# Kernel tuning notes

Measured on AMD Instinct MI355X. Metric: run time of the kernel, lower is better.

Reference implementation:

```python
import jax, jax.numpy as jnp
import numpy as np

HIDDEN_SIZE = 256
INPUT_SIZE = 4
N_CLASSES = 2
START_VALUE_PADDING = -100.0


def setup_inputs() -> dict:
    key = jax.random.key(0)
    ks = jax.random.split(key, 11)
    B, T = 128, 2048
    H, IN = HIDDEN_SIZE, INPUT_SIZE
    s = 1.0 / np.sqrt(H)  # torch LSTM/Linear default init scale
    u = lambda k, shape: jax.random.uniform(k, shape, jnp.float32, -s, s)
    return {
        "y": jax.random.normal(ks[0], (B, T), dtype=jnp.float32),
        "W_ih0": u(ks[1], (4 * H, IN)),
        "W_hh0": u(ks[2], (4 * H, H)),
        "b_ih0": u(ks[3], (4 * H,)),
        "b_hh0": u(ks[4], (4 * H,)),
        "W_ih1": u(ks[5], (4 * H, H)),
        "W_hh1": u(ks[6], (4 * H, H)),
        "b_ih1": u(ks[7], (4 * H,)),
        "b_hh1": u(ks[8], (4 * H,)),
        "W_fc": u(ks[9], (N_CLASSES, H)),
        "b_fc": u(ks[10], (N_CLASSES,)),
    }


def _cell(x, h, c, W_ih, W_hh, b):
    # torch LSTM gate order: i, f, g, o
    g = x @ W_ih.T + h @ W_hh.T + b
    i, f, gg, o = jnp.split(g, 4, axis=-1)
    c = jax.nn.sigmoid(f) * c + jax.nn.sigmoid(i) * jnp.tanh(gg)
    h = jax.nn.sigmoid(o) * jnp.tanh(c)
    return h, c


def reference(y, W_ih0, W_hh0, b_ih0, b_hh0, W_ih1, W_hh1, b_ih1, b_hh1, W_fc, b_fc):
    B, T = y.shape
    H, IN = HIDDEN_SIZE, INPUT_SIZE
    # torch roll-on-padded-array windowing == prepend IN-1 pad values,
    # window t = [y_pre[t], ..., y_pre[t+IN-1]] (oldest-first, current sample last)
    y_pre = jnp.concatenate(
        [jnp.full((B, IN - 1), START_VALUE_PADDING, y.dtype), y], axis=1)
    idx = jnp.arange(T)[:, None] + jnp.arange(IN)[None, :]  # [T, IN]
    seq = y_pre[:, idx]  # [B, T, IN]

    b0 = b_ih0 + b_hh0
    b1 = b_ih1 + b_hh1

    def step(carry, x_t):
        h1, c1, h2, c2 = carry
        h1, c1 = _cell(x_t, h1, c1, W_ih0, W_hh0, b0)
        h2, c2 = _cell(h1, h2, c2, W_ih1, W_hh1, b1)
        return (h1, c1, h2, c2), h2

    z = jnp.zeros((B, H), y.dtype)
    _, hs = jax.lax.scan(step, (z, z, z, z), seq.transpose(1, 0, 2))  # hs: [T,B,H]
    lstm_out = hs.transpose(1, 0, 2)  # [B, T, H]
    out = lstm_out @ W_fc.T + b_fc  # [B, T, N_CLASSES]  (phase='train')
    return out
```

## Files before the change

### kernel.cpp

```cpp
#include <hip/hip_runtime.h>
#include <math.h>

#define T_LEN 2048
#define NTH   512

typedef __attribute__((ext_vector_type(8))) short short8v;
typedef __attribute__((ext_vector_type(4))) float f32x4;
typedef unsigned int u32t;
typedef unsigned long long u64t;

#define H1_OFF  0
#define H2_OFF  131072
#define ABT_OFF 262144
#define WS_U32  262145


__device__ __forceinline__ float fsigm(float x) {
  return __builtin_amdgcn_rcpf(1.0f + __builtin_amdgcn_exp2f(-1.44269504f * x));
}
__device__ __forceinline__ float ftanh(float x) {
  return fmaf(-2.0f, __builtin_amdgcn_rcpf(1.0f + __builtin_amdgcn_exp2f(2.88539009f * x)), 1.0f);
}
__device__ __forceinline__ u32t bf_rn(float x) {
  u32t b; __builtin_memcpy(&b, &x, 4);
  return (b + 0x7FFFu + ((b >> 16) & 1u)) >> 16;
}
__device__ __forceinline__ void split_bf(float x, u32t& hi, u32t& lo) {
  hi = bf_rn(x);
  u32t hb = hi << 16; float hf; __builtin_memcpy(&hf, &hb, 4);
  lo = bf_rn(x - hf);
}

__global__ void init_ws_kernel(u32t* ws) {
  for (int i = blockIdx.x * blockDim.x + threadIdx.x; i < WS_U32;
       i += gridDim.x * blockDim.x)
    ws[i] = (i < ABT_OFF) ? 0x40000000u : 0u;
}

#define MFMA16(a, b, c) __builtin_amdgcn_mfma_f32_16x16x32_bf16(a, b, c, 0, 0, 0)
#define ALD64(ptr) __hip_atomic_load((ptr), __ATOMIC_RELAXED, __HIP_MEMORY_SCOPE_AGENT)
#define ALD32(ptr) __hip_atomic_load((ptr), __ATOMIC_RELAXED, __HIP_MEMORY_SCOPE_AGENT)
#define AST32(ptr, v) __hip_atomic_store((ptr), (v), __ATOMIC_RELAXED, __HIP_MEMORY_SCOPE_AGENT)

__launch_bounds__(NTH, 2)
__global__ void lstm_persist(const float* __restrict__ y,
                             const float* __restrict__ Wih0, const float* __restrict__ Whh0,
                             const float* __restrict__ bih0, const float* __restrict__ bhh0,
                             const float* __restrict__ Wih1, const float* __restrict__ Whh1,
                             const float* __restrict__ bih1, const float* __restrict__ bhh1,
                             const float* __restrict__ Wfc, const float* __restrict__ bfc,
                             float* __restrict__ out, u32t* wsu) {
  extern __shared__ char lds[];
  const int tid   = threadIdx.x;
  const int lane  = tid & 63;
  const int wid   = tid >> 6;
  const int gang  = blockIdx.x >> 4;
  const int slice = blockIdx.x & 15;
  const int gA    = gang;
  const int gB    = gang + 16;

  u32t* h1b    = wsu + H1_OFF;
  u32t* h2b    = wsu + H2_OFF;
  u32t* abortf = wsu + ABT_OFF;

  for (int i = tid; i < 16384; i += NTH) ((u32t*)lds)[i] = 0u;

  const bool isL1 = (wid >= 4);
  const int  m = lane & 15, kq4 = lane >> 4;
  const int  gate = m & 3, hs4 = m >> 2;
  const int  hidb = slice * 16 + (wid & 3) * 4;
  const int  grow = gate * 256 + hidb + hs4;

  const float* WA = isL1 ? Wih1 : Whh0;
  const float* WB = isL1 ? Whh1 : Wfc;
  const int   rowB   = isL1 ? grow : m;
  const bool  bValid = isL1 || (wid == 0 && m < 2);

  short8v ahi[16], alo[16];
  #pragma unroll
  for (int ks = 0; ks < 8; ++ks) {
    short8v h0, l0, h1, l1;
    #pragma unroll
    for (int j = 0; j < 8; ++j) {
      int k = ks * 32 + kq4 * 8 + j;
      u32t hi, lo;
      split_bf(WA[grow * 256 + k], hi, lo);
      h0[j] = (short)hi; l0[j] = (short)lo;
      float vb = bValid ? WB[rowB * 256 + k] : 0.f;
      split_bf(vb, hi, lo);
      h1[j] = (short)hi; l1[j] = (short)lo;
    }
    ahi[ks] = h0;     alo[ks] = l0;
    ahi[8 + ks] = h1; alo[8 + ks] = l1;
  }

  const int hidC = hidb + kq4;
  float bias4[4], wx[16];
  #pragma unroll
  for (int r = 0; r < 4; ++r) {
    int row = r * 256 + hidC;
    bias4[r] = isL1 ? (bih1[row] + bhh1[row]) : (bih0[row] + bhh0[row]);
    #pragma unroll
    for (int kk = 0; kk < 4; ++kk)
      wx[r * 4 + kk] = isL1 ? 0.f : Wih0[row * 4 + kk];
  }
  float bfc0 = 0.f, bfc1 = 0.f;
  if (wid == 0) { bfc0 = bfc[0]; bfc1 = bfc[1]; }
  const float* ybA = y + (gA * 4 + (m & 3)) * T_LEN;
  const float* ybB = y + (gB * 4 + (m & 3)) * T_LEN;

  float cstA = 0.f, cstB = 0.f;

  const int srow = tid >> 7;
  const int sc2  = (tid & 127) * 2;
  const int soff = srow * 512 + (((tid & 127) * 4) ^ (srow << 4));
  const int brow = lane & 15;
  const int bxr  = (brow & 7) << 4;
  const int bco  = kq4 * 16;

#define BRD(sb, pl, ks) \
  (*(const short8v*)((sb) + (pl) * 8192 + brow * 512 + ((((ks) * 64) + bco) ^ bxr)))

  auto section = [&](const char* sbR, char* sbW, int sG, int oG, int sp, int qp,
                     float& cst, const float* yb) {
    const bool act = isL1 ? (sp >= 1 && sp <= T_LEN) : (sp < T_LEN);

    f32x4 accP = {0.f, 0.f, 0.f, 0.f}, accQ = {0.f, 0.f, 0.f, 0.f};
    if (act) {
      if (!isL1) {
        #pragma unroll
        for (int ks = 0; ks < 8; ++ks) {
          short8v bh = BRD(sbR, 0, ks), bl = BRD(sbR, 1, ks);
          accP = MFMA16(ahi[ks], bh, accP);
          accQ = MFMA16(ahi[ks], bl, accQ);
          accQ = MFMA16(alo[ks], bh, accQ);
        }
      } else {
        #pragma unroll
        for (int ks = 0; ks < 8; ++ks) {
          short8v b1h = BRD(sbR, 0, ks), b1l = BRD(sbR, 1, ks);
          short8v b2h = BRD(sbR, 2, ks), b2l = BRD(sbR, 3, ks);
          accP = MFMA16(ahi[ks], b1h, accP);
          accQ = MFMA16(ahi[ks], b1l, accQ);
          accQ = MFMA16(alo[ks], b1h, accQ);
          accP = MFMA16(ahi[8 + ks], b2h, accP);
          accQ = MFMA16(ahi[8 + ks], b2l, accQ);
          accQ = MFMA16(alo[8 + ks], b2h, accQ);
        }
      }
    }

    if (act) {
      float g[4];
      #pragma unroll
      for (int r = 0; r < 4; ++r) g[r] = accP[r] + accQ[r] + bias4[r];
      if (!isL1) {
        float xx[4];
        #pragma unroll
        for (int kk = 0; kk < 4; ++kk) {
          int ti = sp + kk - 3;
          xx[kk] = (ti >= 0) ? yb[ti] : -100.0f;
        }
        #pragma unroll
        for (int kk = 0; kk < 4; ++kk)
          #pragma unroll
          for (int r = 0; r < 4; ++r) g[r] = fmaf(wx[r * 4 + kk], xx[kk], g[r]);
      }
      cst = fsigm(g[1]) * cst + fsigm(g[0]) * ftanh(g[2]);
      float hv = fsigm(g[3]) * ftanh(cst);
      if (m < 4) {
        const int step = isL1 ? (sp - 1) : sp;
        u32t w; __builtin_memcpy(&w, &hv, 4);
        w |= ((u32t)((step >> 2) & 1)) << 30;
        u32t* dst = (isL1 ? h2b : h1b) + (step & 3) * 32768 + sG * 1024 + m * 256 + hidC;
        AST32(dst, w);
      }
    }

    const bool ld1 = (qp >= 1 && qp <= T_LEN);
    const bool ld2 = (qp >= 2 && qp <= T_LEN + 1);
    const u64t* s1 = (const u64t*)(h1b + ((qp - 1) & 3) * 32768 + oG * 1024 + srow * 256 + sc2);
    const u64t* s2 = (const u64t*)(h2b + ((qp - 2) & 3) * 32768 + oG * 1024 + srow * 256 + sc2);
    u64t v1 = 0, v2 = 0;
    if (ld1) v1 = ALD64(s1);
    if (ld2) v2 = ALD64(s2);

    if (wid == 0 && sp >= 2 && slice == ((sp - 2) & 15)) {
      f32x4 aF = {0.f, 0.f, 0.f, 0.f}, aG = {0.f, 0.f, 0.f, 0.f};
      #pragma unroll
      for (int ks = 0; ks < 8; ++ks) {
        short8v b2h = BRD(sbR, 2, ks), b2l = BRD(sbR, 3, ks);
        aF = MFMA16(ahi[8 + ks], b2h, aF);
        aG = MFMA16(ahi[8 + ks], b2l, aG);
        aG = MFMA16(alo[8 + ks], b2h, aG);
      }
      if (lane < 4) {
        float2 o;
        o.x = aF[0] + aG[0] + bfc0;
        o.y = aF[1] + aG[1] + bfc1;
        *(float2*)(&out[(sG * 4 + lane) * (T_LEN * 2) + (sp - 2) * 2]) = o;
      }
    }

    const u32t gb1 = (u32t)(((qp - 1) >> 2) & 1);
    const u32t gb2 = (u32t)(((qp - 2) >> 2) & 1);
    bool ok1 = !ld1 || ((((u32t)v1 >> 30) & 1) == gb1 && (((u32t)(v1 >> 32) >> 30) & 1) == gb1);
    bool ok2 = !ld2 || ((((u32t)v2 >> 30) & 1) == gb2 && (((u32t)(v2 >> 32) >> 30) & 1) == gb2);
    int guard = 0;
    while (!(ok1 && ok2)) {
      __builtin_amdgcn_s_sleep(1);
      if (!ok1) {
        v1 = ALD64(s1);
        ok1 = ((((u32t)v1 >> 30) & 1) == gb1 && (((u32t)(v1 >> 32) >> 30) & 1) == gb1);
      }
      if (!ok2) {
        v2 = ALD64(s2);
        ok2 = ((((u32t)v2 >> 30) & 1) == gb2 && (((u32t)(v2 >> 32) >> 30) & 1) == gb2);
      }
      if (++guard > (1 << 16)) { AST32(abortf, 1u); break; }
      if ((guard & 63) == 0 && ALD32(abortf) != 0) break;
    }

    if (ld1) {
      u32t w0 = (u32t)v1 & 0xBFFFFFFFu, w1 = (u32t)(v1 >> 32) & 0xBFFFFFFFu;
      float f0, f1; __builtin_memcpy(&f0, &w0, 4); __builtin_memcpy(&f1, &w1, 4);
      u32t h0, l0, h1_, l1_;
      split_bf(f0, h0, l0); split_bf(f1, h1_, l1_);
      *(u32t*)(sbW + soff)        = h0 | (h1_ << 16);
      *(u32t*)(sbW + 8192 + soff) = l0 | (l1_ << 16);
    }
    if (ld2) {
      u32t w0 = (u32t)v2 & 0xBFFFFFFFu, w1 = (u32t)(v2 >> 32) & 0xBFFFFFFFu;
      float f0, f1; __builtin_memcpy(&f0, &w0, 4); __builtin_memcpy(&f1, &w1, 4);
      u32t h0, l0, h1_, l1_;
      split_bf(f0, h0, l0); split_bf(f1, h1_, l1_);
      *(u32t*)(sbW + 16384 + soff) = h0 | (h1_ << 16);
      *(u32t*)(sbW + 24576 + soff) = l0 | (l1_ << 16);
    }
    __syncthreads();
  };

  char* LA = lds;
  char* LB = lds + 32768;

  __syncthreads();

  for (int p = 0; p <= T_LEN + 1; ++p) {
    section(LA, LB, gA, gB, p, p, cstA, ybA);
    section(LB, LA, gB, gA, p, p + 1, cstB, ybB);
  }
}

extern "C" void kernel_launch(void* const* d_in, const int* in_sizes, int n_in,
                              void* d_out, int out_size, void* d_ws, size_t ws_size,
                              hipStream_t stream) {
  const float* y    = (const float*)d_in[0];
  const float* Wih0 = (const float*)d_in[1];
  const float* Whh0 = (const float*)d_in[2];
  const float* bih0 = (const float*)d_in[3];
  const float* bhh0 = (const float*)d_in[4];
  const float* Wih1 = (const float*)d_in[5];
  const float* Whh1 = (const float*)d_in[6];
  const float* bih1 = (const float*)d_in[7];
  const float* bhh1 = (const float*)d_in[8];
  const float* Wfc  = (const float*)d_in[9];
  const float* bfc  = (const float*)d_in[10];
  float* out = (float*)d_out;
  u32t*  ws  = (u32t*)d_ws;

  (void)hipFuncSetAttribute(reinterpret_cast<const void*>(lstm_persist),
                            hipFuncAttributeMaxDynamicSharedMemorySize, 131072);

  hipLaunchKernelGGL(init_ws_kernel, dim3(256), dim3(256), 0, stream, ws);
  hipLaunchKernelGGL(lstm_persist, dim3(256), dim3(NTH), 131072, stream,
                     y, Wih0, Whh0, bih0, bhh0, Wih1, Whh1, bih1, bhh1,
                     Wfc, bfc, out, ws);
}
```

Measured before the change: 7.284 ms.

## Restructure persistent LSTM into 8 groups of 16 batch rows, one section per step

```diff
diff --git a/kernel.cpp b/kernel.cpp
--- a/kernel.cpp
+++ b/kernel.cpp
@@ -54,10 +54,8 @@
   const int tid   = threadIdx.x;
   const int lane  = tid & 63;
   const int wid   = tid >> 6;
-  const int gang  = blockIdx.x >> 4;
-  const int slice = blockIdx.x & 15;
-  const int gA    = gang;
-  const int gB    = gang + 16;
+  const int group = blockIdx.x & 7;
+  const int slice = blockIdx.x >> 3;
 
   u32t* h1b    = wsu + H1_OFF;
   u32t* h2b    = wsu + H2_OFF;
@@ -106,24 +104,38 @@
   }
   float bfc0 = 0.f, bfc1 = 0.f;
   if (wid == 0) { bfc0 = bfc[0]; bfc1 = bfc[1]; }
-  const float* ybA = y + (gA * 4 + (m & 3)) * T_LEN;
-  const float* ybB = y + (gB * 4 + (m & 3)) * T_LEN;
-
-  float cstA = 0.f, cstB = 0.f;
-
-  const int srow = tid >> 7;
-  const int sc2  = (tid & 127) * 2;
-  const int soff = srow * 512 + (((tid & 127) * 4) ^ (srow << 4));
+  const float* yb = y + (group * 16 + m) * T_LEN;
+
+  float cst = 0.f;
+
+  const int srow = tid >> 5;
+  const int ch   = tid & 31;
+  const int sc8  = ch * 8;
+  const int soff = srow * 512 + ((ch * 16) ^ ((srow & 7) << 4));
+  const bool own = (ch >> 1) == slice;
   const int brow = lane & 15;
   const int bxr  = (brow & 7) << 4;
   const int bco  = kq4 * 16;
+  const int dwb = m * 512 + ((hidC * 2) ^ ((m & 7) << 4));
 
 #define BRD(sb, pl, ks) \
   (*(const short8v*)((sb) + (pl) * 8192 + brow * 512 + ((((ks) * 64) + bco) ^ bxr)))
 
-  auto section = [&](const char* sbR, char* sbW, int sG, int oG, int sp, int qp,
-                     float& cst, const float* yb) {
-    const bool act = isL1 ? (sp >= 1 && sp <= T_LEN) : (sp < T_LEN);
+  __syncthreads();
+
+  for (int p = 0; p <= T_LEN + 1; ++p) {
+    const char* sbR = lds + (p & 1) * 32768;
+    char*       sbW = lds + ((p & 1) ^ 1) * 32768;
+    const bool act = isL1 ? (p >= 1 && p <= T_LEN) : (p < T_LEN);
+
+    float xx[4];
+    if (!isL1 && p < T_LEN) {
+      #pragma unroll
+      for (int kk = 0; kk < 4; ++kk) {
+        int ti = p + kk - 3;
+        xx[kk] = (ti >= 0) ? yb[ti] : -100.0f;
+      }
+    }
 
     f32x4 accP = {0.f, 0.f, 0.f, 0.f}, accQ = {0.f, 0.f, 0.f, 0.f};
     if (act) {
@@ -155,12 +167,6 @@
       #pragma unroll
       for (int r = 0; r < 4; ++r) g[r] = accP[r] + accQ[r] + bias4[r];
       if (!isL1) {
-        float xx[4];
-        #pragma unroll
-        for (int kk = 0; kk < 4; ++kk) {
-          int ti = sp + kk - 3;
-          xx[kk] = (ti >= 0) ? yb[ti] : -100.0f;
-        }
         #pragma unroll
         for (int kk = 0; kk < 4; ++kk)
           #pragma unroll
@@ -168,24 +174,32 @@
       }
       cst = fsigm(g[1]) * cst + fsigm(g[0]) * ftanh(g[2]);
       float hv = fsigm(g[3]) * ftanh(cst);
-      if (m < 4) {
-        const int step = isL1 ? (sp - 1) : sp;
-        u32t w; __builtin_memcpy(&w, &hv, 4);
-        w |= ((u32t)((step >> 2) & 1)) << 30;
-        u32t* dst = (isL1 ? h2b : h1b) + (step & 3) * 32768 + sG * 1024 + m * 256 + hidC;
-        AST32(dst, w);
-      }
-    }
-
-    const bool ld1 = (qp >= 1 && qp <= T_LEN);
-    const bool ld2 = (qp >= 2 && qp <= T_LEN + 1);
-    const u64t* s1 = (const u64t*)(h1b + ((qp - 1) & 3) * 32768 + oG * 1024 + srow * 256 + sc2);
-    const u64t* s2 = (const u64t*)(h2b + ((qp - 2) & 3) * 32768 + oG * 1024 + srow * 256 + sc2);
-    u64t v1 = 0, v2 = 0;
-    if (ld1) v1 = ALD64(s1);
-    if (ld2) v2 = ALD64(s2);
-
-    if (wid == 0 && sp >= 2 && slice == ((sp - 2) & 15)) {
+      const int step = isL1 ? (p - 1) : p;
+      u32t w; __builtin_memcpy(&w, &hv, 4);
+      w |= ((u32t)((step >> 2) & 1)) << 30;
+      u32t* dst = (isL1 ? h2b : h1b) + (step & 3) * 32768 + group * 4096 + m * 256 + hidC;
+      AST32(dst, w);
+      u32t hi, lo; split_bf(hv, hi, lo);
+      char* base = sbW + (isL1 ? 16384 : 0);
+      *(unsigned short*)(base + dwb)        = (unsigned short)hi;
+      *(unsigned short*)(base + 8192 + dwb) = (unsigned short)lo;
+    }
+
+    const bool ld1 = !own && (p < T_LEN);
+    const bool ld2 = !own && (p >= 1 && p <= T_LEN);
+    const u64t* s1 = (const u64t*)(h1b + (p & 3) * 32768 + group * 4096 + srow * 256 + sc8);
+    const u64t* s2 = (const u64t*)(h2b + ((p - 1) & 3) * 32768 + group * 4096 + srow * 256 + sc8);
+    u64t v1[4], v2[4];
+    if (ld1) {
+      #pragma unroll
+      for (int j = 0; j < 4; ++j) v1[j] = ALD64(s1 + j);
+    }
+    if (ld2) {
+      #pragma unroll
+      for (int j = 0; j < 4; ++j) v2[j] = ALD64(s2 + j);
+    }
+
+    if (wid == 0 && p >= 2 && slice == ((p - 2) & 15)) {
       f32x4 aF = {0.f, 0.f, 0.f, 0.f}, aG = {0.f, 0.f, 0.f, 0.f};
       #pragma unroll
       for (int ks = 0; ks < 8; ++ks) {
@@ -194,60 +208,84 @@
         aG = MFMA16(ahi[8 + ks], b2l, aG);
         aG = MFMA16(alo[8 + ks], b2h, aG);
       }
-      if (lane < 4) {
+      if (lane < 16) {
         float2 o;
         o.x = aF[0] + aG[0] + bfc0;
         o.y = aF[1] + aG[1] + bfc1;
-        *(float2*)(&out[(sG * 4 + lane) * (T_LEN * 2) + (sp - 2) * 2]) = o;
-      }
-    }
-
-    const u32t gb1 = (u32t)(((qp - 1) >> 2) & 1);
-    const u32t gb2 = (u32t)(((qp - 2) >> 2) & 1);
-    bool ok1 = !ld1 || ((((u32t)v1 >> 30) & 1) == gb1 && (((u32t)(v1 >> 32) >> 30) & 1) == gb1);
-    bool ok2 = !ld2 || ((((u32t)v2 >> 30) & 1) == gb2 && (((u32t)(v2 >> 32) >> 30) & 1) == gb2);
-    int guard = 0;
-    while (!(ok1 && ok2)) {
-      __builtin_amdgcn_s_sleep(1);
-      if (!ok1) {
-        v1 = ALD64(s1);
-        ok1 = ((((u32t)v1 >> 30) & 1) == gb1 && (((u32t)(v1 >> 32) >> 30) & 1) == gb1);
-      }
-      if (!ok2) {
-        v2 = ALD64(s2);
-        ok2 = ((((u32t)v2 >> 30) & 1) == gb2 && (((u32t)(v2 >> 32) >> 30) & 1) == gb2);
-      }
-      if (++guard > (1 << 16)) { AST32(abortf, 1u); break; }
-      if ((guard & 63) == 0 && ALD32(abortf) != 0) break;
+        *(float2*)(&out[(group * 16 + lane) * (T_LEN * 2) + (p - 2) * 2]) = o;
+      }
+    }
+
+    {
+      const u32t g1 = (u32t)((p >> 2) & 1);
+      const u32t g2 = (u32t)(((p - 1) >> 2) & 1);
+      u32t st1 = 0, st2 = 0;
+      if (ld1) {
+        #pragma unroll
+        for (int j = 0; j < 4; ++j)
+          if ((((u32t)(v1[j] >> 30)) & 1) != g1 || (((u32t)(v1[j] >> 62)) & 1) != g1)
+            st1 |= 1u << j;
+      }
+      if (ld2) {
+        #pragma unroll
+        for (int j = 0; j < 4; ++j)
+          if ((((u32t)(v2[j] >> 30)) & 1) != g2 || (((u32t)(v2[j] >> 62)) & 1) != g2)
+            st2 |= 1u << j;
+      }
+      int guard = 0;
+      while (st1 | st2) {
+        #pragma unroll
+        for (int j = 0; j < 4; ++j)
+          if (st1 & (1u << j)) v1[j] = ALD64(s1 + j);
+        #pragma unroll
+        for (int j = 0; j < 4; ++j)
+          if (st2 & (1u << j)) v2[j] = ALD64(s2 + j);
+        u32t n1 = 0, n2 = 0;
+        #pragma unroll
+        for (int j = 0; j < 4; ++j)
+          if ((st1 & (1u << j)) &&
+              ((((u32t)(v1[j] >> 30)) & 1) != g1 || (((u32t)(v1[j] >> 62)) & 1) != g1))
+            n1 |= 1u << j;
+        #pragma unroll
+        for (int j = 0; j < 4; ++j)
+          if ((st2 & (1u << j)) &&
+              ((((u32t)(v2[j] >> 30)) & 1) != g2 || (((u32t)(v2[j] >> 62)) & 1) != g2))
+            n2 |= 1u << j;
+        st1 = n1; st2 = n2;
+        if (st1 | st2) {
+          if (++guard > (1 << 16)) { AST32(abortf, 1u); break; }
+          if ((guard & 63) == 0 && ALD32(abortf) != 0) break;
+          if (guard & 1) __builtin_amdgcn_s_sleep(1);
+        }
+      }
     }
 
     if (ld1) {
-      u32t w0 = (u32t)v1 & 0xBFFFFFFFu, w1 = (u32t)(v1 >> 32) & 0xBFFFFFFFu;
-      float f0, f1; __builtin_memcpy(&f0, &w0, 4); __builtin_memcpy(&f1, &w1, 4);
-      u32t h0, l0, h1_, l1_;
-      split_bf(f0, h0, l0); split_bf(f1, h1_, l1_);
-      *(u32t*)(sbW + soff)        = h0 | (h1_ << 16);
-      *(u32t*)(sbW + 8192 + soff) = l0 | (l1_ << 16);
+      short8v vh, vl;
+      #pragma unroll
+      for (int j = 0; j < 8; ++j) {
+        u32t wv = ((u32t)(v1[j >> 1] >> ((j & 1) * 32))) & 0xBFFFFFFFu;
+        float f; __builtin_memcpy(&f, &wv, 4);
+        u32t hi, lo; split_bf(f, hi, lo);
+        vh[j] = (short)hi; vl[j] = (short)lo;
+      }
+      *(short8v*)(sbW + soff)        = vh;
+      *(short8v*)(sbW + 8192 + soff) = vl;
     }
     if (ld2) {
-      u32t w0 = (u32t)v2 & 0xBFFFFFFFu, w1 = (u32t)(v2 >> 32) & 0xBFFFFFFFu;
-      float f0, f1; __builtin_memcpy(&f0, &w0, 4); __builtin_memcpy(&f1, &w1, 4);
-      u32t h0, l0, h1_, l1_;
-      split_bf(f0, h0, l0); split_bf(f1, h1_, l1_);
-      *(u32t*)(sbW + 16384 + soff) = h0 | (h1_ << 16);
-      *(u32t*)(sbW + 24576 + soff) = l0 | (l1_ << 16);
-    }
+      short8v vh, vl;
+      #pragma unroll
+      for (int j = 0; j < 8; ++j) {
+        u32t wv = ((u32t)(v2[j >> 1] >> ((j & 1) * 32))) & 0xBFFFFFFFu;
+        float f; __builtin_memcpy(&f, &wv, 4);
+        u32t hi, lo; split_bf(f, hi, lo);
+        vh[j] = (short)hi; vl[j] = (short)lo;
+      }
+      *(short8v*)(sbW + 16384 + soff) = vh;
+      *(short8v*)(sbW + 24576 + soff) = vl;
+    }
+
     __syncthreads();
-  };
-
-  char* LA = lds;
-  char* LB = lds + 32768;
-
-  __syncthreads();
-
-  for (int p = 0; p <= T_LEN + 1; ++p) {
-    section(LA, LB, gA, gB, p, p, cstA, ybA);
-    section(LB, LA, gB, gA, p, p + 1, cstB, ybB);
   }
 }
 
@@ -272,7 +310,7 @@
                             hipFuncAttributeMaxDynamicSharedMemorySize, 131072);
 
   hipLaunchKernelGGL(init_ws_kernel, dim3(256), dim3(256), 0, stream, ws);
-  hipLaunchKernelGGL(lstm_persist, dim3(256), dim3(NTH), 131072, stream,
+  hipLaunchKernelGGL(lstm_persist, dim3(128), dim3(NTH), 131072, stream,
                      y, Wih0, Whh0, bih0, bhh0, Wih1, Whh1, bih1, bhh1,
                      Wfc, bfc, out, ws);
 }
```

Result: slower. 21.00 ms (+188.3%).
